# Kernel optimization log

Hardware: AMD Instinct MI355X
Metric: run time of the kernel (lower is better)

## Reference

```python
import jax, jax.numpy as jnp
import numpy as np
import math

B, T, C, H = 4, 1024, 1024, 16
D = C // H  # head dim = 64

def setup_inputs() -> dict:
    key = jax.random.key(0)
    ks = jax.random.split(key, 10)
    s = 1.0 / math.sqrt(C)
    x = jax.random.normal(ks[0], (B, T, C), dtype=jnp.float32)
    pad = (jax.random.uniform(ks[1], (B, T)) < 0.2).astype(jnp.float32)
    # ensure first token of every row is unpadded so softmax rows are well-posed
    pad = pad.at[:, 0].set(0.0)
    Wq = jax.random.normal(ks[2], (C, C), dtype=jnp.float32) * s
    bq = jnp.zeros((C,), dtype=jnp.float32)
    Wk = jax.random.normal(ks[3], (C, C), dtype=jnp.float32) * s
    bk = jnp.zeros((C,), dtype=jnp.float32)
    Wv = jax.random.normal(ks[4], (C, C), dtype=jnp.float32) * s
    bv = jnp.zeros((C,), dtype=jnp.float32)
    Wp = jax.random.normal(ks[5], (C, C), dtype=jnp.float32) * s
    bp = jnp.zeros((C,), dtype=jnp.float32)
    return {"x": x, "x_padding_judge": pad, "Wq": Wq, "bq": bq,
            "Wk": Wk, "bk": bk, "Wv": Wv, "bv": bv, "Wp": Wp, "bp": bp}

def reference(x, x_padding_judge, Wq, bq, Wk, bk, Wv, bv, Wp, bp):
    # keep flag: 1.0 where token is real, 0.0 where padded
    keep = 1.0 - x_padding_judge                      # [B, T]
    mask = keep[:, :, None] * keep[:, None, :]        # [B, T, T] outer product
    # projections, split heads: [B, H, T, D]
    def heads(w, b):
        return (x @ w + b).reshape(B, T, H, D).transpose(0, 2, 1, 3)
    q, k, v = heads(Wq, bq), heads(Wk, bk), heads(Wv, bv)
    att = jnp.einsum('bhqd,bhkd->bhqk', q, k) * (1.0 / math.sqrt(D))
    # attn_pdrop=0 => att_full is all ones; masked_fill where mask == 0
    att = jnp.where(mask[:, None, :, :] == 0, -1e9, att)
    att = jax.nn.softmax(att, axis=-1)
    y = jnp.einsum('bhqk,bhkd->bhqd', att, v)         # [B, H, T, D]
    y = y.transpose(0, 2, 1, 3).reshape(B, T, C)
    return y @ Wp + bp
```

## Files before the change

kernel.cpp:

```cpp
#include <hip/hip_runtime.h>
#include <hip/hip_bf16.h>
#include <math.h>

#define Bb 4
#define Tt 1024
#define Cc 1024
#define Hh 16
#define Dd 64

typedef __attribute__((ext_vector_type(8))) _Float16 half8;
typedef __attribute__((ext_vector_type(4))) _Float16 half4;
typedef __attribute__((ext_vector_type(4))) float floatx4;


__device__ __forceinline__ void gload_lds16(const _Float16* g, const _Float16* l)
{
    __builtin_amdgcn_global_load_lds(
        (const __attribute__((address_space(1))) void*)g,
        (__attribute__((address_space(3))) void*)l, 16, 0, 0);
}

struct PrepP { const float* x; _Float16* xh; const float* W[4]; _Float16* out[4]; };

__global__ __launch_bounds__(256) void prep_all(PrepP p)
{
    if (blockIdx.x < 256) {
        const int m16 = blockIdx.x;
        const int r   = threadIdx.x & 15;
        const int kc0 = threadIdx.x >> 4;
        const float* src = p.x + (size_t)(m16 * 16 + r) * 1024;
        _Float16*   dst = p.xh + (size_t)m16 * 16384 + r * 8;
#pragma unroll
        for (int c8 = 0; c8 < 8; ++c8) {
            const int kc = kc0 + c8 * 16;
            float4 a = *(const float4*)(src + kc * 8);
            float4 b = *(const float4*)(src + kc * 8 + 4);
            half8 h;
            h[0] = (_Float16)a.x; h[1] = (_Float16)a.y; h[2] = (_Float16)a.z; h[3] = (_Float16)a.w;
            h[4] = (_Float16)b.x; h[5] = (_Float16)b.y; h[6] = (_Float16)b.z; h[7] = (_Float16)b.w;
            *(half8*)(dst + kc * 128) = h;
        }
        return;
    }
    const int bid2 = blockIdx.x - 256;
    const int z    = bid2 >> 8;
    const int rem  = bid2 & 255;
    const int n0   = (rem & 15) * 64;
    const int k0   = (rem >> 4) * 64;
    const float* __restrict__ W = p.W[z];
    _Float16* __restrict__ outp = p.out[z];
    __shared__ float tile[64][65];
    const int tr  = threadIdx.x >> 4;
    const int tc4 = (threadIdx.x & 15) * 4;

#pragma unroll
    for (int i = 0; i < 4; ++i) {
        const int kk = tr + i * 16;
        float4 v = *(const float4*)(W + (size_t)(k0 + kk) * 1024 + n0 + tc4);
        tile[kk][tc4 + 0] = v.x;
        tile[kk][tc4 + 1] = v.y;
        tile[kk][tc4 + 2] = v.z;
        tile[kk][tc4 + 3] = v.w;
    }
    __syncthreads();
#pragma unroll
    for (int i = 0; i < 4; ++i) {
        half4 h;
#pragma unroll
        for (int c = 0; c < 4; ++c) h[c] = (_Float16)tile[tc4 + c][tr + i * 16];
        _Float16* dst = outp + (size_t)((n0 >> 4) + i) * 16384
                        + ((k0 + tc4) >> 3) * 128 + tr * 8 + (tc4 & 7);
        *(half4*)dst = h;
    }
}

struct QkvP { const _Float16* Wt[3]; const float* bias[3];
              _Float16* qb; _Float16* kb; _Float16* vt; };

#define QKV_STEP(CUR, SBUF, TS, DOSTAGE, TAILWAIT)                          \
    {                                                                       \
        half8 af[2], bf[4];                                                 \
        _Pragma("unroll")                                                   \
        for (int i = 0; i < 2; ++i)                                         \
            af[i] = *(const half8*)&As[CUR][wr * 2 + i][lane * 8];          \
        _Pragma("unroll")                                                   \
        for (int j = 0; j < 4; ++j)                                         \
            bf[j] = *(const half8*)&Bs[CUR][wc * 4 + j][lane * 8];          \
        if (DOSTAGE) {                                                      \
            const size_t ko = (size_t)(TS) * 512;                           \
            gload_lds16(ga + ko, &As[SBUF][w][0]);                          \
            gload_lds16(gb + ko, &Bs[SBUF][w][0]);                          \
        }                                                                   \
        _Pragma("unroll")                                                   \
        for (int i = 0; i < 2; ++i)                                         \
            _Pragma("unroll")                                               \
            for (int j = 0; j < 4; ++j)                                     \
                acc[i][j] = __builtin_amdgcn_mfma_f32_16x16x32_f16(         \
                    af[i], bf[j], acc[i][j], 0, 0, 0);                      \
        if ((TAILWAIT) == 2)                                                \
            asm volatile("s_waitcnt vmcnt(2)" ::: "memory");                \
        else if ((TAILWAIT) == 0)                                           \
            asm volatile("s_waitcnt vmcnt(0)" ::: "memory");                \
        if ((TAILWAIT) >= 0) __builtin_amdgcn_s_barrier();                  \
    }

__global__ __launch_bounds__(512) void gemm_qkv(const _Float16* __restrict__ xh, QkvP p)
{
    const int z = blockIdx.z;
    const _Float16* __restrict__ Wt   = p.Wt[z];
    const float* __restrict__    bias = p.bias[z];

    const int tid  = threadIdx.x;
    const int lane = tid & 63;
    const int w    = tid >> 6;
    const int wr   = w >> 1, wc = w & 1;
    const int quad = lane >> 4;
    const int l15  = lane & 15;
    const int bm   = blockIdx.x * 128;
    const int bn   = blockIdx.y * 128;

    __shared__ __align__(16) _Float16 As[3][8][512];
    __shared__ __align__(16) _Float16 Bs[3][8][512];

    const _Float16* ga = xh + (size_t)((bm >> 4) + w) * 16384 + lane * 8;
    const _Float16* gb = Wt + (size_t)((bn >> 4) + w) * 16384 + lane * 8;

    floatx4 acc[2][4];
#pragma unroll
    for (int i = 0; i < 2; ++i)
#pragma unroll
        for (int j = 0; j < 4; ++j)
            acc[i][j] = (floatx4){0.f, 0.f, 0.f, 0.f};

    gload_lds16(ga, &As[0][w][0]);
    gload_lds16(gb, &Bs[0][w][0]);
    gload_lds16(ga + 512, &As[1][w][0]);
    gload_lds16(gb + 512, &Bs[1][w][0]);
    asm volatile("s_waitcnt vmcnt(2)" ::: "memory");
    __builtin_amdgcn_s_barrier();

    for (int tt = 0; tt < 30; tt += 3) {
        QKV_STEP(0, 2, tt + 2, true, 2);
        QKV_STEP(1, 0, tt + 3, true, 2);
        QKV_STEP(2, 1, tt + 4, true, 2);
    }
    QKV_STEP(0, 0, 0, false, 0);
    QKV_STEP(1, 0, 0, false, -1);

    if (z == 2) {
#pragma unroll
        for (int j = 0; j < 4; ++j) {
            const int col = bn + wc * 64 + j * 16 + l15;
            const int h  = col >> 6;
            const float bj = bias[col];
#pragma unroll
            for (int i = 0; i < 2; ++i) {
                const int t0 = bm + wr * 32 + i * 16 + quad * 4;
                const int bh = (t0 >> 10) * 16 + h;
                const int tm = t0 & 1023;
                half4 pk;
#pragma unroll
                for (int r = 0; r < 4; ++r) pk[r] = (_Float16)(acc[i][j][r] + bj);
                *(half4*)(p.vt + (size_t)bh * 65536 + (size_t)j * 16384
                          + (tm >> 3) * 128 + l15 * 8 + (tm & 7)) = pk;
            }
        }
    } else {
        _Float16* outp = (z == 0) ? p.qb : p.kb;
#pragma unroll
        for (int j = 0; j < 4; ++j) {
            const int col = bn + wc * 64 + j * 16 + l15;
            const int h  = col >> 6;
            const int dd = col & 63;
            const float bj = bias[col];
            const int doff = (dd >> 3) * 128 + (dd & 7);
#pragma unroll
            for (int i = 0; i < 2; ++i) {
#pragma unroll
                for (int r = 0; r < 4; ++r) {
                    const int tg = bm + wr * 32 + i * 16 + quad * 4 + r;
                    const int bh = (tg >> 10) * 16 + h;
                    const int tm = tg & 1023;
                    outp[(size_t)bh * 65536 + (tm >> 4) * 1024 + doff + (tm & 15) * 8] =
                        (_Float16)(acc[i][j][r] + bj);
                }
            }
        }
    }
}

#define ATTN_STEP(CUR, SBUF, TC, TS, DOSTAGE, TAILWAIT)                     \
    {                                                                       \
        half8 ak[2][4], bv[2][4];                                           \
        _Pragma("unroll")                                                   \
        for (int ks = 0; ks < 2; ++ks)                                      \
            _Pragma("unroll")                                               \
            for (int mk = 0; mk < 4; ++mk)                                  \
                ak[ks][mk] = *(const half8*)&Ks[CUR][mk * 2 + ks][lane * 8];\
        _Pragma("unroll")                                                   \
        for (int ks = 0; ks < 2; ++ks)                                      \
            _Pragma("unroll")                                               \
            for (int dj = 0; dj < 4; ++dj)                                  \
                bv[ks][dj] = *(const half8*)&Vs[CUR][dj * 2 + ks][lane * 8];\
        if (DOSTAGE) {                                                      \
            _Pragma("unroll")                                               \
            for (int c = 0; c < 2; ++c) {                                   \
                const int f = w * 2 + c;                                    \
                gload_lds16(kf + (size_t)((TS) * 4 + (f >> 1)) * 1024       \
                            + (f & 1) * 512 + lane * 8, &Ks[SBUF][f][0]);   \
                gload_lds16(vf + (size_t)(f >> 1) * 16384                   \
                            + (size_t)(TS) * 1024 + (f & 1) * 512           \
                            + lane * 8, &Vs[SBUF][f][0]);                   \
            }                                                               \
        }                                                                   \
        float4 kk4[4];                                                      \
        _Pragma("unroll")                                                   \
        for (int mk = 0; mk < 4; ++mk)                                      \
            kk4[mk] = *(const float4*)&Pad[(TC) * 64 + mk * 16 + quad * 4]; \
        floatx4 ST[4][2];                                                   \
        _Pragma("unroll")                                                   \
        for (int mk = 0; mk < 4; ++mk)                                      \
            _Pragma("unroll")                                               \
            for (int nq = 0; nq < 2; ++nq)                                  \
                ST[mk][nq] = (floatx4){0.f, 0.f, 0.f, 0.f};                 \
        _Pragma("unroll")                                                   \
        for (int ks = 0; ks < 2; ++ks)                                      \
            _Pragma("unroll")                                               \
            for (int mk = 0; mk < 4; ++mk)                                  \
                _Pragma("unroll")                                           \
                for (int nq = 0; nq < 2; ++nq)                              \
                    ST[mk][nq] = __builtin_amdgcn_mfma_f32_16x16x32_f16(    \
                        ak[ks][mk], bq[ks][nq], ST[mk][nq], 0, 0, 0);       \
        _Pragma("unroll")                                                   \
        for (int mk = 0; mk < 4; ++mk) {                                    \
            const float kkr[4] = {1.0f - kk4[mk].x, 1.0f - kk4[mk].y,       \
                                  1.0f - kk4[mk].z, 1.0f - kk4[mk].w};      \
            _Pragma("unroll")                                               \
            for (int nq = 0; nq < 2; ++nq) {                                \
                half4 pk;                                                   \
                _Pragma("unroll")                                           \
                for (int r = 0; r < 4; ++r) {                               \
                    const float e = __builtin_amdgcn_exp2f(ST[mk][nq][r] * SC); \
                    const float pv = (kq[nq] == 0.0f) ? 1.0f : kkr[r] * e;  \
                    pk[r] = (_Float16)pv;                                   \
                }                                                           \
                *(half4*)&Ps[w][((mk * 2 + (quad >> 1)) * 32 + nq * 16 + l15) * 8 \
                               + (quad & 1) * 4] = pk;                      \
            }                                                               \
        }                                                                   \
        _Pragma("unroll")                                                   \
        for (int ks = 0; ks < 2; ++ks) {                                    \
            half8 ap[2];                                                    \
            _Pragma("unroll")                                               \
            for (int mi = 0; mi < 2; ++mi)                                  \
                ap[mi] = *(const half8*)&Ps[w][((ks * 4 + quad) * 32 + mi * 16 + l15) * 8]; \
            _Pragma("unroll")                                               \
            for (int mi = 0; mi < 2; ++mi) {                                \
                _Pragma("unroll")                                           \
                for (int dj = 0; dj < 4; ++dj)                              \
                    O[mi][dj] = __builtin_amdgcn_mfma_f32_16x16x32_f16(     \
                        ap[mi], bv[ks][dj], O[mi][dj], 0, 0, 0);            \
                l_acc[mi] = __builtin_amdgcn_mfma_f32_16x16x32_f16(         \
                    ap[mi], ones, l_acc[mi], 0, 0, 0);                      \
            }                                                               \
        }                                                                   \
        if ((TAILWAIT) == 4)                                                \
            asm volatile("s_waitcnt vmcnt(4)" ::: "memory");                \
        else if ((TAILWAIT) == 0)                                           \
            asm volatile("s_waitcnt vmcnt(0)" ::: "memory");                \
        if ((TAILWAIT) >= 0) __builtin_amdgcn_s_barrier();                  \
    }

__global__ __launch_bounds__(256) void attn_mfma(
    const _Float16* __restrict__ qb, const _Float16* __restrict__ kb,
    const _Float16* __restrict__ vt, const float* __restrict__ padj,
    _Float16* __restrict__ yh)
{
    __shared__ __align__(16) _Float16 Ps[4][2048];
    __shared__ __align__(16) _Float16 Ks[3][8][512];
    __shared__ __align__(16) _Float16 Vs[3][8][512];
    __shared__ __align__(16) float    Pad[1024];

    const int tid  = threadIdx.x;
    const int lane = tid & 63;
    const int w    = tid >> 6;
    const int quad = lane >> 4;
    const int l15  = lane & 15;
    const int bh   = blockIdx.x;
    const int q0   = blockIdx.y * 128;
    const int b    = bh >> 4;
    const int h    = bh & 15;

    const _Float16* qf = qb + (size_t)bh * 65536;
    const _Float16* kf = kb + (size_t)bh * 65536;
    const _Float16* vf = vt + (size_t)bh * 65536;
    const float*    pk_row = padj + b * Tt;

    *(float4*)&Pad[tid * 4] = *(const float4*)(pk_row + tid * 4);

    half8 bq[2][2];
#pragma unroll
    for (int ks = 0; ks < 2; ++ks)
#pragma unroll
        for (int nq = 0; nq < 2; ++nq)
            bq[ks][nq] = *(const half8*)(qf + (size_t)((q0 >> 4) + w * 2 + nq) * 1024
                                         + ks * 512 + lane * 8);
    float kq[2];
#pragma unroll
    for (int nq = 0; nq < 2; ++nq)
        kq[nq] = 1.0f - pk_row[q0 + w * 32 + nq * 16 + l15];

    floatx4 O[2][4];
    floatx4 l_acc[2];
#pragma unroll
    for (int mi = 0; mi < 2; ++mi) {
#pragma unroll
        for (int dj = 0; dj < 4; ++dj) O[mi][dj] = (floatx4){0.f, 0.f, 0.f, 0.f};
        l_acc[mi] = (floatx4){0.f, 0.f, 0.f, 0.f};
    }
    half8 ones;
#pragma unroll
    for (int j = 0; j < 8; ++j) ones[j] = (_Float16)1.0f;

    constexpr float SC = 0.18033688011112042f;

    __syncthreads();

#pragma unroll
    for (int tb = 0; tb < 2; ++tb) {
#pragma unroll
        for (int c = 0; c < 2; ++c) {
            const int f = w * 2 + c;
            gload_lds16(kf + (size_t)(tb * 4 + (f >> 1)) * 1024
                        + (f & 1) * 512 + lane * 8, &Ks[tb][f][0]);
            gload_lds16(vf + (size_t)(f >> 1) * 16384 + (size_t)tb * 1024
                        + (f & 1) * 512 + lane * 8, &Vs[tb][f][0]);
        }
    }
    asm volatile("s_waitcnt vmcnt(4)" ::: "memory");
    __builtin_amdgcn_s_barrier();

    for (int tt = 0; tt < 12; tt += 3) {
        ATTN_STEP(0, 2, tt + 0, tt + 2, true, 4);
        ATTN_STEP(1, 0, tt + 1, tt + 3, true, 4);
        ATTN_STEP(2, 1, tt + 2, tt + 4, true, 4);
    }
    ATTN_STEP(0, 2, 12, 14, true, 4);
    ATTN_STEP(1, 0, 13, 15, true, 4);
    ATTN_STEP(2, 0, 14, 0, false, 0);
    ATTN_STEP(0, 0, 15, 0, false, -1);

#pragma unroll
    for (int mi = 0; mi < 2; ++mi) {
#pragma unroll
        for (int r = 0; r < 4; ++r) {
            const int rowl  = w * 32 + mi * 16 + quad * 4 + r;
            const int token = b * Tt + q0 + rowl;
            const float inv = 1.0f / l_acc[mi][r];
            const size_t tb = (size_t)(token >> 4) * 16384 + (token & 15) * 8;
#pragma unroll
            for (int dj = 0; dj < 4; ++dj) {
                const int col = h * 64 + dj * 16 + l15;
                yh[tb + (col >> 3) * 128 + (col & 7)] = (_Float16)(O[mi][dj][r] * inv);
            }
        }
    }
}

#define PROJ_STEP(CUR, SBUF, TS, DOSTAGE, TAILWAIT)                         \
    {                                                                       \
        half8 af[2], bf[4];                                                 \
        _Pragma("unroll")                                                   \
        for (int i = 0; i < 2; ++i)                                         \
            af[i] = *(const half8*)&As[CUR][wr * 2 + i][lane * 8];          \
        _Pragma("unroll")                                                   \
        for (int j = 0; j < 4; ++j)                                         \
            bf[j] = *(const half8*)&Bs[CUR][wc * 4 + j][lane * 8];          \
        if (DOSTAGE) {                                                      \
            const size_t ko = (size_t)(TS) * 512;                           \
            gload_lds16(ga + ko, &As[SBUF][w][0]);                          \
            gload_lds16(gb + ko, &Bs[SBUF][w][0]);                          \
        }                                                                   \
        _Pragma("unroll")                                                   \
        for (int i = 0; i < 2; ++i)                                         \
            _Pragma("unroll")                                               \
            for (int j = 0; j < 4; ++j)                                     \
                acc[i][j] = __builtin_amdgcn_mfma_f32_16x16x32_f16(         \
                    af[i], bf[j], acc[i][j], 0, 0, 0);                      \
        if ((TAILWAIT) == 6)                                                \
            asm volatile("s_waitcnt vmcnt(6)" ::: "memory");                \
        else if ((TAILWAIT) == 4)                                           \
            asm volatile("s_waitcnt vmcnt(4)" ::: "memory");                \
        else if ((TAILWAIT) == 2)                                           \
            asm volatile("s_waitcnt vmcnt(2)" ::: "memory");                \
        else if ((TAILWAIT) == 0)                                           \
            asm volatile("s_waitcnt vmcnt(0)" ::: "memory");                \
        if ((TAILWAIT) >= 0) __builtin_amdgcn_s_barrier();                  \
    }

__global__ __launch_bounds__(512) void gemm_proj(const _Float16* __restrict__ Ay,
                                                 const _Float16* __restrict__ Bt,
                                                 const float* __restrict__ bias,
                                                 float* __restrict__ out)
{
    const int tid  = threadIdx.x;
    const int lane = tid & 63;
    const int w    = tid >> 6;
    const int wr   = w >> 1, wc = w & 1;
    const int quad = lane >> 4;
    const int l15  = lane & 15;
    const int bm   = blockIdx.x * 128;
    const int bn   = blockIdx.y * 128;

    __shared__ __align__(16) _Float16 As[5][8][512];
    __shared__ __align__(16) _Float16 Bs[5][8][512];

    const _Float16* ga = Ay + (size_t)((bm >> 4) + w) * 16384 + lane * 8;
    const _Float16* gb = Bt + (size_t)((bn >> 4) + w) * 16384 + lane * 8;

    floatx4 acc[2][4];
#pragma unroll
    for (int i = 0; i < 2; ++i)
#pragma unroll
        for (int j = 0; j < 4; ++j)
            acc[i][j] = (floatx4){0.f, 0.f, 0.f, 0.f};

#pragma unroll
    for (int tb = 0; tb < 4; ++tb) {
        gload_lds16(ga + (size_t)tb * 512, &As[tb][w][0]);
        gload_lds16(gb + (size_t)tb * 512, &Bs[tb][w][0]);
    }
    asm volatile("s_waitcnt vmcnt(6)" ::: "memory");
    __builtin_amdgcn_s_barrier();

    for (int tt = 0; tt < 25; tt += 5) {
        PROJ_STEP(0, 4, tt + 4, true, 6);
        PROJ_STEP(1, 0, tt + 5, true, 6);
        PROJ_STEP(2, 1, tt + 6, true, 6);
        PROJ_STEP(3, 2, tt + 7, true, 6);
        PROJ_STEP(4, 3, tt + 8, true, 6);
    }
    PROJ_STEP(0, 4, 29, true, 6);
    PROJ_STEP(1, 0, 30, true, 6);
    PROJ_STEP(2, 1, 31, true, 6);
    PROJ_STEP(3, 0, 0, false, 4);
    PROJ_STEP(4, 0, 0, false, 2);
    PROJ_STEP(0, 0, 0, false, 0);
    PROJ_STEP(1, 0, 0, false, -1);

#pragma unroll
    for (int j = 0; j < 4; ++j) {
        const int col = bn + wc * 64 + j * 16 + l15;
        const float bj = bias[col];
#pragma unroll
        for (int i = 0; i < 2; ++i) {
            const int row = bm + wr * 32 + i * 16 + quad * 4;
            float* o = out + (size_t)row * 1024 + col;
#pragma unroll
            for (int r = 0; r < 4; ++r)
                o[(size_t)r * 1024] = acc[i][j][r] + bj;
        }
    }
}

extern "C" void kernel_launch(void* const* d_in, const int* in_sizes, int n_in,
                              void* d_out, int out_size, void* d_ws, size_t ws_size,
                              hipStream_t stream)
{
    const float* x    = (const float*)d_in[0];
    const float* padj = (const float*)d_in[1];
    const float* Wq   = (const float*)d_in[2];
    const float* bq   = (const float*)d_in[3];
    const float* Wk   = (const float*)d_in[4];
    const float* bk   = (const float*)d_in[5];
    const float* Wv   = (const float*)d_in[6];
    const float* bv   = (const float*)d_in[7];
    const float* Wp   = (const float*)d_in[8];
    const float* bp   = (const float*)d_in[9];
    float* out = (float*)d_out;

    const size_t MB = 1024 * 1024;
    char* ws = (char*)d_ws;
    _Float16* xh  = (_Float16*)(ws);
    _Float16* Wt0 = (_Float16*)(ws +  8 * MB);
    _Float16* Wt1 = (_Float16*)(ws + 10 * MB);
    _Float16* Wt2 = (_Float16*)(ws + 12 * MB);
    _Float16* Wtp = (_Float16*)(ws + 14 * MB);
    _Float16* qb  = (_Float16*)(ws + 16 * MB);
    _Float16* kb  = (_Float16*)(ws + 24 * MB);
    _Float16* vtb = (_Float16*)(ws + 32 * MB);
    _Float16* yh  = (_Float16*)(ws + 40 * MB);

    PrepP pp;
    pp.x = x; pp.xh = xh;
    pp.W[0] = Wq; pp.W[1] = Wk; pp.W[2] = Wv; pp.W[3] = Wp;
    pp.out[0] = Wt0; pp.out[1] = Wt1; pp.out[2] = Wt2; pp.out[3] = Wtp;
    prep_all<<<1280, 256, 0, stream>>>(pp);

    QkvP qp;
    qp.Wt[0] = Wt0; qp.Wt[1] = Wt1; qp.Wt[2] = Wt2;
    qp.bias[0] = bq; qp.bias[1] = bk; qp.bias[2] = bv;
    qp.qb = qb; qp.kb = kb; qp.vt = vtb;
    gemm_qkv<<<dim3(32, 8, 3), 512, 0, stream>>>(xh, qp);

    attn_mfma<<<dim3(64, 8), 256, 0, stream>>>(qb, kb, vtb, padj, yh);

    gemm_proj<<<dim3(32, 8), 512, 0, stream>>>(yh, Wtp, bp, out);
}
```

Before: 177.7 us.

## Replace LDS-staged K/V pipeline with direct global-to-register double buffering

The attention kernel no longer stages K and V tiles through shared memory with global_load_lds, waitcnt and block barriers. Each wave now loads its K/V fragments straight from global memory into two register buffers, prefetching the next tile while computing the current one. Pad flags are read directly from global memory instead of an LDS copy. This removes the barriers and LDS traffic, but all four waves now load the same K/V data redundantly from global/L2. It also raises register pressure, which may lower occupancy.

After: 190.1 us. +7.0%, slower.

```diff
diff --git a/kernel.cpp b/kernel.cpp
--- a/kernel.cpp
+++ b/kernel.cpp
@@ -189,34 +189,26 @@
     }
 }
 
-#define ATTN_STEP(CUR, SBUF, TC, TS, DOSTAGE, TAILWAIT)                     \
+#define ATTN_TILE(AKC, BVC, AKN, BVN, KTC, KTN, DOLOAD)                     \
     {                                                                       \
-        half8 ak[2][4], bv[2][4];                                           \
-        _Pragma("unroll")                                                   \
-        for (int ks = 0; ks < 2; ++ks)                                      \
-            _Pragma("unroll")                                               \
-            for (int mk = 0; mk < 4; ++mk)                                  \
-                ak[ks][mk] = *(const half8*)&Ks[CUR][mk * 2 + ks][lane * 8];\
-        _Pragma("unroll")                                                   \
-        for (int ks = 0; ks < 2; ++ks)                                      \
-            _Pragma("unroll")                                               \
-            for (int dj = 0; dj < 4; ++dj)                                  \
-                bv[ks][dj] = *(const half8*)&Vs[CUR][dj * 2 + ks][lane * 8];\
-        if (DOSTAGE) {                                                      \
-            _Pragma("unroll")                                               \
-            for (int c = 0; c < 2; ++c) {                                   \
-                const int f = w * 2 + c;                                    \
-                gload_lds16(kf + (size_t)((TS) * 4 + (f >> 1)) * 1024       \
-                            + (f & 1) * 512 + lane * 8, &Ks[SBUF][f][0]);   \
-                gload_lds16(vf + (size_t)(f >> 1) * 16384                   \
-                            + (size_t)(TS) * 1024 + (f & 1) * 512           \
-                            + lane * 8, &Vs[SBUF][f][0]);                   \
+        if (DOLOAD) {                                                       \
+            _Pragma("unroll")                                               \
+            for (int ks = 0; ks < 2; ++ks) {                                \
+                _Pragma("unroll")                                           \
+                for (int mk = 0; mk < 4; ++mk)                              \
+                    AKN[ks][mk] = *(const half8*)(kf                        \
+                        + (size_t)(((KTN) >> 4) + mk) * 1024                \
+                        + ks * 512 + lane * 8);                             \
+                _Pragma("unroll")                                           \
+                for (int dj = 0; dj < 4; ++dj)                              \
+                    BVN[ks][dj] = *(const half8*)(vf + (size_t)dj * 16384   \
+                        + ((KTN) >> 3) * 128 + ks * 512 + lane * 8);        \
             }                                                               \
         }                                                                   \
         float4 kk4[4];                                                      \
         _Pragma("unroll")                                                   \
         for (int mk = 0; mk < 4; ++mk)                                      \
-            kk4[mk] = *(const float4*)&Pad[(TC) * 64 + mk * 16 + quad * 4]; \
+            kk4[mk] = *(const float4*)(pk_row + (KTC) + mk * 16 + quad * 4);\
         floatx4 ST[4][2];                                                   \
         _Pragma("unroll")                                                   \
         for (int mk = 0; mk < 4; ++mk)                                      \
@@ -230,7 +222,7 @@
                 _Pragma("unroll")                                           \
                 for (int nq = 0; nq < 2; ++nq)                              \
                     ST[mk][nq] = __builtin_amdgcn_mfma_f32_16x16x32_f16(    \
-                        ak[ks][mk], bq[ks][nq], ST[mk][nq], 0, 0, 0);       \
+                        AKC[ks][mk], bq[ks][nq], ST[mk][nq], 0, 0, 0);      \
         _Pragma("unroll")                                                   \
         for (int mk = 0; mk < 4; ++mk) {                                    \
             const float kkr[4] = {1.0f - kk4[mk].x, 1.0f - kk4[mk].y,       \
@@ -259,16 +251,11 @@
                 _Pragma("unroll")                                           \
                 for (int dj = 0; dj < 4; ++dj)                              \
                     O[mi][dj] = __builtin_amdgcn_mfma_f32_16x16x32_f16(     \
-                        ap[mi], bv[ks][dj], O[mi][dj], 0, 0, 0);            \
+                        ap[mi], BVC[ks][dj], O[mi][dj], 0, 0, 0);           \
                 l_acc[mi] = __builtin_amdgcn_mfma_f32_16x16x32_f16(         \
                     ap[mi], ones, l_acc[mi], 0, 0, 0);                      \
             }                                                               \
         }                                                                   \
-        if ((TAILWAIT) == 4)                                                \
-            asm volatile("s_waitcnt vmcnt(4)" ::: "memory");                \
-        else if ((TAILWAIT) == 0)                                           \
-            asm volatile("s_waitcnt vmcnt(0)" ::: "memory");                \
-        if ((TAILWAIT) >= 0) __builtin_amdgcn_s_barrier();                  \
     }
 
 __global__ __launch_bounds__(256) void attn_mfma(
@@ -277,9 +264,6 @@
     _Float16* __restrict__ yh)
 {
     __shared__ __align__(16) _Float16 Ps[4][2048];
-    __shared__ __align__(16) _Float16 Ks[3][8][512];
-    __shared__ __align__(16) _Float16 Vs[3][8][512];
-    __shared__ __align__(16) float    Pad[1024];
 
     const int tid  = threadIdx.x;
     const int lane = tid & 63;
@@ -296,8 +280,6 @@
     const _Float16* vf = vt + (size_t)bh * 65536;
     const float*    pk_row = padj + b * Tt;
 
-    *(float4*)&Pad[tid * 4] = *(const float4*)(pk_row + tid * 4);
-
     half8 bq[2][2];
 #pragma unroll
     for (int ks = 0; ks < 2; ++ks)
@@ -324,31 +306,23 @@
 
     constexpr float SC = 0.18033688011112042f;
 
-    __syncthreads();
-
-#pragma unroll
-    for (int tb = 0; tb < 2; ++tb) {
-#pragma unroll
-        for (int c = 0; c < 2; ++c) {
-            const int f = w * 2 + c;
-            gload_lds16(kf + (size_t)(tb * 4 + (f >> 1)) * 1024
-                        + (f & 1) * 512 + lane * 8, &Ks[tb][f][0]);
-            gload_lds16(vf + (size_t)(f >> 1) * 16384 + (size_t)tb * 1024
-                        + (f & 1) * 512 + lane * 8, &Vs[tb][f][0]);
-        }
-    }
-    asm volatile("s_waitcnt vmcnt(4)" ::: "memory");
-    __builtin_amdgcn_s_barrier();
-
-    for (int tt = 0; tt < 12; tt += 3) {
-        ATTN_STEP(0, 2, tt + 0, tt + 2, true, 4);
-        ATTN_STEP(1, 0, tt + 1, tt + 3, true, 4);
-        ATTN_STEP(2, 1, tt + 2, tt + 4, true, 4);
-    }
-    ATTN_STEP(0, 2, 12, 14, true, 4);
-    ATTN_STEP(1, 0, 13, 15, true, 4);
-    ATTN_STEP(2, 0, 14, 0, false, 0);
-    ATTN_STEP(0, 0, 15, 0, false, -1);
+    half8 ak0[2][4], bv0[2][4], ak1[2][4], bv1[2][4];
+#pragma unroll
+    for (int ks = 0; ks < 2; ++ks) {
+#pragma unroll
+        for (int mk = 0; mk < 4; ++mk)
+            ak0[ks][mk] = *(const half8*)(kf + (size_t)mk * 1024 + ks * 512 + lane * 8);
+#pragma unroll
+        for (int dj = 0; dj < 4; ++dj)
+            bv0[ks][dj] = *(const half8*)(vf + (size_t)dj * 16384 + ks * 512 + lane * 8);
+    }
+
+    for (int tt = 0; tt < 896; tt += 128) {
+        ATTN_TILE(ak0, bv0, ak1, bv1, tt, tt + 64, true);
+        ATTN_TILE(ak1, bv1, ak0, bv0, tt + 64, tt + 128, true);
+    }
+    ATTN_TILE(ak0, bv0, ak1, bv1, 896, 960, true);
+    ATTN_TILE(ak1, bv1, ak0, bv0, 960, 0, false);
 
 #pragma unroll
     for (int mi = 0; mi < 2; ++mi) {
```
